# Optimization experiments

Hardware: AMD Instinct MI355X
Metric: run time of the kernel (lower is better)

Reference implementation:

```python
import jax, jax.numpy as jnp
import numpy as np

B1, B2 = 4096, 4096
DF, MF = 1024, 512
H1, H2, H3, H1_ = 2048, 1024, 512, 1024
DO, MO = 1, 1


def _lin(x, W, b):
    return x @ W.T + b


def setup_inputs() -> dict:
    key = jax.random.key(0)
    ks = jax.random.split(key, 22)

    def w(k, o, i):
        return (jax.random.normal(k, (o, i), jnp.float32) / np.sqrt(i)).astype(jnp.float32)

    def bz(k, o):
        return jax.random.normal(k, (o,), jnp.float32) * 0.01

    return {
        'x1': jax.random.normal(ks[0], (B1, DF), jnp.float32),
        'x2': jax.random.normal(ks[1], (B2, MF), jnp.float32),
        'W1_1': w(ks[2], H1, DF),  'b1_1': bz(ks[3], H1),
        'W1_2': w(ks[4], H2, H1),  'b1_2': bz(ks[5], H2),
        'W1_3': w(ks[6], H3, H2),  'b1_3': bz(ks[7], H3),
        'W1_4': w(ks[8], H2, H3),  'b1_4': bz(ks[9], H2),
        'W1_5': w(ks[10], H1, H2), 'b1_5': bz(ks[11], H1),
        'Wp1':  w(ks[12], DO, H1), 'bp1':  bz(ks[13], DO),
        'W2_1': w(ks[14], H1_, MF), 'b2_1': bz(ks[15], H1_),
        'W2_2': w(ks[16], H3, H1_), 'b2_2': bz(ks[17], H3),
        'W2_3': w(ks[18], H1_, H3), 'b2_3': bz(ks[19], H1_),
        'Wp2':  w(ks[20], MO, H1_), 'bp2':  bz(ks[21], MO),
    }


def reference(x1, x2, W1_1, b1_1, W1_2, b1_2, W1_3, b1_3, W1_4, b1_4,
              W1_5, b1_5, Wp1, bp1, W2_1, b2_1, W2_2, b2_2, W2_3, b2_3,
              Wp2, bp2):
    # dropout: eval mode (identity)
    h = jax.nn.relu(_lin(x1, W1_1, b1_1))
    h = jax.nn.relu(_lin(h, W1_2, b1_2))
    x_1 = jax.nn.sigmoid(_lin(h, W1_3, b1_3))          # [B1, H3]
    h = jax.nn.relu(_lin(x_1, W1_4, b1_4))
    h = jax.nn.relu(_lin(h, W1_5, b1_5))
    x2_1 = jax.nn.sigmoid(_lin(h, Wp1, bp1))           # [B1, DO]

    g = jax.nn.relu(_lin(x2, W2_1, b2_1))
    x_2 = jax.nn.sigmoid(_lin(g, W2_2, b2_2))          # [B2, H3]
    g = jax.nn.relu(_lin(x_2, W2_3, b2_3))
    x2_2 = jax.nn.sigmoid(_lin(g, Wp2, bp2))           # [B2, MO]

    # Python loop over x_1 rows doing (x_2 * row).sum(1) == single GEMM x_1 @ x_2.T
    scores = x_1 @ x_2.T                                # [B1, B2]
    pre_dm = scores.reshape(-1)                         # row-major matches torch.cat order
    # MinMaxScaler.fit_transform on detached values (original uses .data -> no grad)
    pre_dm = jax.lax.stop_gradient(pre_dm)
    mn, mx = pre_dm.min(), pre_dm.max()
    pre_dm = (pre_dm - mn) / (mx - mn)

    pre_data = x2_1.reshape(-1)
    pre_model = x2_2.T.reshape(-1)
    return (pre_data, pre_dm, pre_model)
```

## Files before the change

kernel.cpp:

```cpp
#include <hip/hip_runtime.h>
#include <hip/hip_bf16.h>

typedef __bf16 bf16_t;
typedef bf16_t bf16x8 __attribute__((ext_vector_type(8)));
typedef bf16_t bf16x4 __attribute__((ext_vector_type(4)));
typedef float f32x4 __attribute__((ext_vector_type(4)));

typedef __attribute__((address_space(1))) const void gconst_void;
typedef __attribute__((address_space(3))) void lds_void;

__device__ __forceinline__ void async16(const bf16_t* g, bf16_t* l) {
  __builtin_amdgcn_global_load_lds((gconst_void*)g, (lds_void*)l, 16, 0, 0);
}

struct CvtDesc { const float* src; bf16_t* dst; long n; };
struct CvtArgs { CvtDesc d[10]; };

__global__ __launch_bounds__(256) void cvt_many(CvtArgs a) {
  const CvtDesc de = a.d[blockIdx.y];
  long i = ((long)blockIdx.x * 256 + threadIdx.x) * 4;
  const long stride = (long)gridDim.x * 256 * 4;
  for (; i < de.n; i += stride) {
    float4 v = *(const float4*)(de.src + i);
    bf16x4 o;
    o[0] = (bf16_t)v.x; o[1] = (bf16_t)v.y; o[2] = (bf16_t)v.z; o[3] = (bf16_t)v.w;
    *(bf16x4*)(de.dst + i) = o;
  }
}

struct GDesc {
  const bf16_t* A; const bf16_t* W; const float* bias; void* C;
  int N, K, act;
};
struct GArgs { GDesc d[2]; int ntiles0; };

template <typename OutT, bool MINMAX>
__global__ __launch_bounds__(256) void gemm_gb(GArgs ga, float* __restrict__ pmin,
                                               float* __restrict__ pmax) {
  const int b = blockIdx.x;
  const int p = (b >= ga.ntiles0) ? 1 : 0;
  const GDesc d = ga.d[p];
  const int local = b - (p ? ga.ntiles0 : 0);
  const int bm = (local & 31) * 128;
  const int bn = (local >> 5) * 128;
  const int N = d.N, K = d.K;

  __shared__ __align__(16) bf16_t As[2][128 * 32];
  __shared__ __align__(16) bf16_t Bs[2][128 * 32];

  const int t = threadIdx.x;
  const int wave = t >> 6;
  const int lane = t & 63;
  const int quad = lane >> 4;
  const int l15 = lane & 15;
  const int wm = (wave >> 1) * 64;
  const int wn = (wave & 1) * 64;

  f32x4 acc[4][4];
#pragma unroll
  for (int i = 0; i < 4; ++i)
#pragma unroll
    for (int j = 0; j < 4; ++j) acc[i][j] = (f32x4){0.f, 0.f, 0.f, 0.f};

  const int c0 = t, c1 = t + 256;
  const int r0 = c0 >> 2, kc0 = ((c0 & 3) - r0) & 3;
  const int r1 = c1 >> 2, kc1 = ((c1 & 3) - r1) & 3;
  const bf16_t* pa0 = d.A + (long)(bm + r0) * K + kc0 * 8;
  const bf16_t* pa1 = d.A + (long)(bm + r1) * K + kc1 * 8;
  const bf16_t* pw0 = d.W + (long)(bn + r0) * K + kc0 * 8;
  const bf16_t* pw1 = d.W + (long)(bn + r1) * K + kc1 * 8;
  bf16_t* lA0 = &As[0][c0 * 8]; bf16_t* lA1 = &As[0][c1 * 8];
  bf16_t* lB0 = &Bs[0][c0 * 8]; bf16_t* lB1 = &Bs[0][c1 * 8];
  const int bufOff = 128 * 32;

  async16(pa0, lA0); async16(pa1, lA1);
  async16(pw0, lB0); async16(pw1, lB1);

  int buf = 0;
  for (int k0 = 0; k0 < K; k0 += 32) {
    __syncthreads();
    const int kn = k0 + 32;
    if (kn < K) {
      const int o = (buf ^ 1) * bufOff;
      async16(pa0 + kn, lA0 + o); async16(pa1 + kn, lA1 + o);
      async16(pw0 + kn, lB0 + o); async16(pw1 + kn, lB1 + o);
    }
    const bf16_t* as = As[buf];
    const bf16_t* bs = Bs[buf];
    bf16x8 af[4], bfr[4];
#pragma unroll
    for (int i = 0; i < 4; ++i) {
      const int r = wm + i * 16 + l15;
      af[i] = *(const bf16x8*)&as[r * 32 + ((quad + r) & 3) * 8];
    }
#pragma unroll
    for (int j = 0; j < 4; ++j) {
      const int r = wn + j * 16 + l15;
      bfr[j] = *(const bf16x8*)&bs[r * 32 + ((quad + r) & 3) * 8];
    }
#pragma unroll
    for (int i = 0; i < 4; ++i)
#pragma unroll
      for (int j = 0; j < 4; ++j)
        acc[i][j] = __builtin_amdgcn_mfma_f32_16x16x32_bf16(af[i], bfr[j],
                                                            acc[i][j], 0, 0, 0);
    buf ^= 1;
  }

  OutT* C = (OutT*)d.C;
  const int row0 = bm + wm + quad * 4;
  const int col0 = bn + wn + l15;
  float mn = 3.4e38f, mx = -3.4e38f;
#pragma unroll
  for (int j = 0; j < 4; ++j) {
    const int col = col0 + j * 16;
    const float bv = d.bias ? d.bias[col] : 0.f;
#pragma unroll
    for (int i = 0; i < 4; ++i) {
#pragma unroll
      for (int r = 0; r < 4; ++r) {
        float v = acc[i][j][r] + bv;
        if (d.act == 1) v = fmaxf(v, 0.f);
        else if (d.act == 2) v = 1.f / (1.f + expf(-v));
        C[(long)(row0 + i * 16 + r) * N + col] = (OutT)v;
        if (MINMAX) { mn = fminf(mn, v); mx = fmaxf(mx, v); }
      }
    }
  }
  if (MINMAX) {
#pragma unroll
    for (int off = 32; off > 0; off >>= 1) {
      mn = fminf(mn, __shfl_down(mn, off));
      mx = fmaxf(mx, __shfl_down(mx, off));
    }
    __shared__ float smn[4], smx[4];
    if (lane == 0) { smn[wave] = mn; smx[wave] = mx; }
    __syncthreads();
    if (t == 0) {
      pmin[blockIdx.x] = fminf(fminf(smn[0], smn[1]), fminf(smn[2], smn[3]));
      pmax[blockIdx.x] = fmaxf(fmaxf(smx[0], smx[1]), fmaxf(smx[2], smx[3]));
    }
  }
}

struct RDesc { const bf16_t* A; const float* w; const float* b; float* out; int K; };

__global__ __launch_bounds__(64) void rowdot2(RDesc d0, RDesc d1) {
  const RDesc d = blockIdx.y ? d1 : d0;
  const int row = blockIdx.x;
  const int lane = threadIdx.x;
  const bf16_t* a = d.A + (long)row * d.K;
  float s = 0.f;
  for (int k = lane * 8; k < d.K; k += 64 * 8) {
    bf16x8 av = *(const bf16x8*)&a[k];
    float4 w0 = *(const float4*)&d.w[k];
    float4 w1 = *(const float4*)&d.w[k + 4];
    s += (float)av[0] * w0.x + (float)av[1] * w0.y +
         (float)av[2] * w0.z + (float)av[3] * w0.w +
         (float)av[4] * w1.x + (float)av[5] * w1.y +
         (float)av[6] * w1.z + (float)av[7] * w1.w;
  }
#pragma unroll
  for (int off = 32; off > 0; off >>= 1) s += __shfl_down(s, off);
  if (lane == 0) d.out[row] = 1.f / (1.f + expf(-(s + d.b[0])));
}

__global__ __launch_bounds__(256) void minmax_final(
    const float* __restrict__ pmin, const float* __restrict__ pmax, int nb,
    float* __restrict__ res) {
  float mn = 3.4e38f, mx = -3.4e38f;
  for (int i = threadIdx.x; i < nb; i += 256) {
    mn = fminf(mn, pmin[i]);
    mx = fmaxf(mx, pmax[i]);
  }
#pragma unroll
  for (int off = 32; off > 0; off >>= 1) {
    mn = fminf(mn, __shfl_down(mn, off));
    mx = fmaxf(mx, __shfl_down(mx, off));
  }
  __shared__ float smn[4], smx[4];
  const int wv = threadIdx.x >> 6, ln = threadIdx.x & 63;
  if (ln == 0) { smn[wv] = mn; smx[wv] = mx; }
  __syncthreads();
  if (threadIdx.x == 0) {
    float m0 = fminf(fminf(smn[0], smn[1]), fminf(smn[2], smn[3]));
    float m1 = fmaxf(fmaxf(smx[0], smx[1]), fmaxf(smx[2], smx[3]));
    res[0] = m0;
    res[1] = 1.f / (m1 - m0);
  }
}

__global__ __launch_bounds__(256) void normalize_k(
    float* __restrict__ out, const float* __restrict__ res, long n) {
  const float mn = res[0], inv = res[1];
  long i = ((long)blockIdx.x * 256 + threadIdx.x) * 4;
  const long stride = (long)gridDim.x * 256 * 4;
  for (; i < n; i += stride) {
    float4 v = *(const float4*)&out[i];
    v.x = (v.x - mn) * inv;
    v.y = (v.y - mn) * inv;
    v.z = (v.z - mn) * inv;
    v.w = (v.w - mn) * inv;
    *(float4*)&out[i] = v;
  }
}

extern "C" void kernel_launch(void* const* d_in, const int* in_sizes, int n_in,
                              void* d_out, int out_size, void* d_ws,
                              size_t ws_size, hipStream_t stream) {
  const float* x1   = (const float*)d_in[0];
  const float* x2   = (const float*)d_in[1];
  const float* W1_1 = (const float*)d_in[2];   const float* b1_1 = (const float*)d_in[3];
  const float* W1_2 = (const float*)d_in[4];   const float* b1_2 = (const float*)d_in[5];
  const float* W1_3 = (const float*)d_in[6];   const float* b1_3 = (const float*)d_in[7];
  const float* W1_4 = (const float*)d_in[8];   const float* b1_4 = (const float*)d_in[9];
  const float* W1_5 = (const float*)d_in[10];  const float* b1_5 = (const float*)d_in[11];
  const float* Wp1  = (const float*)d_in[12];  const float* bp1  = (const float*)d_in[13];
  const float* W2_1 = (const float*)d_in[14];  const float* b2_1 = (const float*)d_in[15];
  const float* W2_2 = (const float*)d_in[16];  const float* b2_2 = (const float*)d_in[17];
  const float* W2_3 = (const float*)d_in[18];  const float* b2_3 = (const float*)d_in[19];
  const float* Wp2  = (const float*)d_in[20];  const float* bp2  = (const float*)d_in[21];

  float* out = (float*)d_out;
  float* out_pre_data  = out;
  float* out_pre_dm    = out + 4096;
  float* out_pre_model = out + 4096 + (long)4096 * 4096;

  char* arena = (char*)out_pre_dm;
  const size_t MB = 1024 * 1024;
  bf16_t* x1b   = (bf16_t*)(arena);
  bf16_t* x2b   = (bf16_t*)(arena + 8 * MB);
  bf16_t* W1_1b = (bf16_t*)(arena + 12 * MB);
  bf16_t* W1_2b = (bf16_t*)(arena + 16 * MB);
  bf16_t* W1_3b = (bf16_t*)(arena + 20 * MB);
  bf16_t* W1_4b = (bf16_t*)(arena + 21 * MB);
  bf16_t* W1_5b = (bf16_t*)(arena + 22 * MB);
  bf16_t* W2_1b = (bf16_t*)(arena + 26 * MB);
  bf16_t* W2_2b = (bf16_t*)(arena + 27 * MB);
  bf16_t* W2_3b = (bf16_t*)(arena + 28 * MB);
  bf16_t* bufA  = (bf16_t*)(arena + 32 * MB);
  bf16_t* bufB  = (bf16_t*)(arena + 48 * MB);
  bf16_t* bufC  = (bf16_t*)(arena + 56 * MB);

  char* ws = (char*)d_ws;
  bf16_t* bufX1 = (bf16_t*)(ws);
  bf16_t* bufX2 = (bf16_t*)(ws + 4 * MB);
  float* pmin = (float*)(ws + 8 * MB);
  float* pmax = pmin + 1024;
  float* res  = pmax + 1024;

  CvtArgs ca;
  ca.d[0] = {x1,   x1b,   (long)4096 * 1024};
  ca.d[1] = {x2,   x2b,   (long)4096 * 512};
  ca.d[2] = {W1_1, W1_1b, (long)2048 * 1024};
  ca.d[3] = {W1_2, W1_2b, (long)1024 * 2048};
  ca.d[4] = {W1_3, W1_3b, (long)512 * 1024};
  ca.d[5] = {W1_4, W1_4b, (long)1024 * 512};
  ca.d[6] = {W1_5, W1_5b, (long)2048 * 1024};
  ca.d[7] = {W2_1, W2_1b, (long)1024 * 512};
  ca.d[8] = {W2_2, W2_2b, (long)512 * 1024};
  ca.d[9] = {W2_3, W2_3b, (long)1024 * 512};
  cvt_many<<<dim3(192, 10), 256, 0, stream>>>(ca);

  const long nS = (long)4096 * 4096;
  GArgs g;

  g.d[0] = {x1b, W1_1b, b1_1, bufA, 2048, 1024, 1};
  g.d[1] = {x2b, W2_1b, b2_1, bufC, 1024, 512, 1};
  g.ntiles0 = 512;
  gemm_gb<bf16_t, false><<<768, 256, 0, stream>>>(g, nullptr, nullptr);

  g.d[0] = {bufA, W1_2b, b1_2, bufB, 1024, 2048, 1};
  g.d[1] = {bufC, W2_2b, b2_2, bufX2, 512, 1024, 2};
  g.ntiles0 = 256;
  gemm_gb<bf16_t, false><<<384, 256, 0, stream>>>(g, nullptr, nullptr);

  g.d[0] = {bufB, W1_3b, b1_3, bufX1, 512, 1024, 2};
  g.d[1] = {bufX2, W2_3b, b2_3, bufC, 1024, 512, 1};
  g.ntiles0 = 128;
  gemm_gb<bf16_t, false><<<384, 256, 0, stream>>>(g, nullptr, nullptr);

  g.d[0] = {bufX1, W1_4b, b1_4, bufB, 1024, 512, 1};
  g.d[1] = g.d[0];
  g.ntiles0 = 256;
  gemm_gb<bf16_t, false><<<256, 256, 0, stream>>>(g, nullptr, nullptr);

  g.d[0] = {bufB, W1_5b, b1_5, bufA, 2048, 1024, 1};
  g.d[1] = g.d[0];
  g.ntiles0 = 512;
  gemm_gb<bf16_t, false><<<512, 256, 0, stream>>>(g, nullptr, nullptr);

  RDesc r0 = {bufA, Wp1, bp1, out_pre_data, 2048};
  RDesc r1 = {bufC, Wp2, bp2, out_pre_model, 1024};
  rowdot2<<<dim3(4096, 2), 64, 0, stream>>>(r0, r1);

  g.d[0] = {bufX1, bufX2, nullptr, out_pre_dm, 4096, 512, 0};
  g.d[1] = g.d[0];
  g.ntiles0 = 1024;
  gemm_gb<float, true><<<1024, 256, 0, stream>>>(g, pmin, pmax);

  minmax_final<<<1, 256, 0, stream>>>(pmin, pmax, 1024, res);
  normalize_k<<<2048, 256, 0, stream>>>(out_pre_dm, res, nS);
}
```

Before: 360.5 us.

## Triple-buffer GEMM LDS tiles with partial vmcnt waits for deeper prefetch

```diff
diff --git a/kernel.cpp b/kernel.cpp
--- a/kernel.cpp
+++ b/kernel.cpp
@@ -12,6 +12,9 @@
 __device__ __forceinline__ void async16(const bf16_t* g, bf16_t* l) {
   __builtin_amdgcn_global_load_lds((gconst_void*)g, (lds_void*)l, 16, 0, 0);
 }
+
+#define WAIT_VM4() __builtin_amdgcn_s_waitcnt(0xF74)
+#define WAIT_VM0() __builtin_amdgcn_s_waitcnt(0xF70)
 
 struct CvtDesc { const float* src; bf16_t* dst; long n; };
 struct CvtArgs { CvtDesc d[10]; };
@@ -44,9 +47,11 @@
   const int bm = (local & 31) * 128;
   const int bn = (local >> 5) * 128;
   const int N = d.N, K = d.K;
-
-  __shared__ __align__(16) bf16_t As[2][128 * 32];
-  __shared__ __align__(16) bf16_t Bs[2][128 * 32];
+  const int NK = K >> 5;
+
+  const int SB = 128 * 32;
+  __shared__ __align__(16) bf16_t As[3 * 128 * 32];
+  __shared__ __align__(16) bf16_t Bs[3 * 128 * 32];
 
   const int t = threadIdx.x;
   const int wave = t >> 6;
@@ -69,24 +74,26 @@
   const bf16_t* pa1 = d.A + (long)(bm + r1) * K + kc1 * 8;
   const bf16_t* pw0 = d.W + (long)(bn + r0) * K + kc0 * 8;
   const bf16_t* pw1 = d.W + (long)(bn + r1) * K + kc1 * 8;
-  bf16_t* lA0 = &As[0][c0 * 8]; bf16_t* lA1 = &As[0][c1 * 8];
-  bf16_t* lB0 = &Bs[0][c0 * 8]; bf16_t* lB1 = &Bs[0][c1 * 8];
-  const int bufOff = 128 * 32;
-
-  async16(pa0, lA0); async16(pa1, lA1);
-  async16(pw0, lB0); async16(pw1, lB1);
-
-  int buf = 0;
-  for (int k0 = 0; k0 < K; k0 += 32) {
-    __syncthreads();
-    const int kn = k0 + 32;
-    if (kn < K) {
-      const int o = (buf ^ 1) * bufOff;
-      async16(pa0 + kn, lA0 + o); async16(pa1 + kn, lA1 + o);
-      async16(pw0 + kn, lB0 + o); async16(pw1 + kn, lB1 + o);
-    }
-    const bf16_t* as = As[buf];
-    const bf16_t* bs = Bs[buf];
+  bf16_t* lA0 = &As[c0 * 8]; bf16_t* lA1 = &As[c1 * 8];
+  bf16_t* lB0 = &Bs[c0 * 8]; bf16_t* lB1 = &Bs[c1 * 8];
+
+  async16(pa0, lA0);            async16(pa1, lA1);
+  async16(pw0, lB0);            async16(pw1, lB1);
+  async16(pa0 + 32, lA0 + SB);  async16(pa1 + 32, lA1 + SB);
+  async16(pw0 + 32, lB0 + SB);  async16(pw1 + 32, lB1 + SB);
+
+  int cs = 0;
+  int ps = 2 * SB;
+  for (int k = 0; k < NK; ++k) {
+    if (k < NK - 1) WAIT_VM4(); else WAIT_VM0();
+    __builtin_amdgcn_s_barrier();
+    if (k + 2 < NK) {
+      const int ko = (k + 2) * 32;
+      async16(pa0 + ko, lA0 + ps); async16(pa1 + ko, lA1 + ps);
+      async16(pw0 + ko, lB0 + ps); async16(pw1 + ko, lB1 + ps);
+    }
+    const bf16_t* as = As + cs;
+    const bf16_t* bs = Bs + cs;
     bf16x8 af[4], bfr[4];
 #pragma unroll
     for (int i = 0; i < 4; ++i) {
@@ -104,7 +111,8 @@
       for (int j = 0; j < 4; ++j)
         acc[i][j] = __builtin_amdgcn_mfma_f32_16x16x32_bf16(af[i], bfr[j],
                                                             acc[i][j], 0, 0, 0);
-    buf ^= 1;
+    cs += SB; if (cs == 3 * SB) cs = 0;
+    ps += SB; if (ps == 3 * SB) ps = 0;
   }
 
   OutT* C = (OutT*)d.C;
```

After: 364.7 us. About the same (+1.2%).
